# Kernel optimization log

Measured on AMD Instinct MI355X. Metric: run time of the kernel, lower is better.

Reference implementation:

```python
import jax, jax.numpy as jnp
import numpy as np

HEAD_DIM = 64
N_KV_HEADS = 4


def _rope(t, cos, sin):
    # t: (B, S, H, HD); cos/sin: (S, HD//2); interleaved (real, imag) pairs
    tr = t.astype(jnp.float32).reshape(*t.shape[:-1], -1, 2)
    xr, xi = tr[..., 0], tr[..., 1]
    c = cos[None, :, None, :]
    s = sin[None, :, None, :]
    out_r = xr * c - xi * s
    out_i = xr * s + xi * c
    return jnp.stack([out_r, out_i], axis=-1).reshape(t.shape).astype(t.dtype)


def setup_inputs() -> dict:
    key = jax.random.key(0)
    ks = jax.random.split(key, 5)
    B, S, D = 2, 2048, 1024
    kv_dim = N_KV_HEADS * HEAD_DIM  # 256
    x = jax.random.normal(ks[0], (B, S, D), jnp.float32)
    wq = jax.random.normal(ks[1], (D, D), jnp.float32) * 0.02
    wk = jax.random.normal(ks[2], (kv_dim, D), jnp.float32) * 0.02
    wv = jax.random.normal(ks[3], (kv_dim, D), jnp.float32) * 0.02
    wo = jax.random.normal(ks[4], (D, D), jnp.float32) * 0.02
    # precompute_freqs_cis (LLaMA): theta = 10000
    half = HEAD_DIM // 2
    inv_freq = 1.0 / (10000.0 ** (np.arange(0, HEAD_DIM, 2).astype(np.float32) / HEAD_DIM))
    ang = np.outer(np.arange(S, dtype=np.float32), inv_freq)  # (S, half)
    freqs_cos = jnp.asarray(np.cos(ang), jnp.float32)
    freqs_sin = jnp.asarray(np.sin(ang), jnp.float32)
    return {"x": x, "wq": wq, "wk": wk, "wv": wv, "wo": wo,
            "freqs_cos": freqs_cos, "freqs_sin": freqs_sin}


def reference(x, wq, wk, wv, wo, freqs_cos, freqs_sin):
    B, S, D = x.shape
    HD = HEAD_DIM
    HKV = N_KV_HEADS
    H = D // HD
    NREP = H // HKV
    # QKV projections (torch Linear: y = x @ W.T)
    xq = jnp.einsum('bsd,od->bso', x, wq).reshape(B, S, H, HD)
    xk = jnp.einsum('bsd,od->bso', x, wk).reshape(B, S, HKV, HD)
    xv = jnp.einsum('bsd,od->bso', x, wv).reshape(B, S, HKV, HD)
    # RoPE (complex multiply on interleaved pairs)
    xq = _rope(xq, freqs_cos, freqs_sin)
    xk = _rope(xk, freqs_cos, freqs_sin)
    # GQA: group query heads by kv head instead of materializing repeated KV
    xq = xq.reshape(B, S, HKV, NREP, HD)
    scale = 1.0 / jnp.sqrt(jnp.asarray(HD, jnp.float32))
    scores = jnp.einsum('bqkrh,bskh->bkrqs', xq, xk) * scale  # (B,HKV,NREP,S,S)
    causal = jnp.tril(jnp.ones((S, S), bool))
    scores = jnp.where(causal, scores, jnp.finfo(scores.dtype).min)
    probs = jax.nn.softmax(scores, axis=-1)
    out = jnp.einsum('bkrqs,bskh->bqkrh', probs, xv).reshape(B, S, H * HD)
    return jnp.einsum('bso,do->bsd', out, wo)
```

## Files before the change

kernel.cpp:

```cpp
#include <hip/hip_runtime.h>
#include <hip/hip_bf16.h>

typedef __attribute__((ext_vector_type(8))) short short8;
typedef __attribute__((ext_vector_type(4))) float floatx4;
typedef __attribute__((ext_vector_type(4))) float float4v;
typedef __attribute__((ext_vector_type(4))) unsigned short ushort4v;

#define S_LEN 2048
#define D_MODEL 1024
#define HD 64
#define HQ 16
#define HKV 4
#define QK_PRESCALE 0.18033688011112042f

__device__ __forceinline__ unsigned short f2bf(float f) {
    unsigned int u = __builtin_bit_cast(unsigned int, f);
    u += 0x7fffu + ((u >> 16) & 1u);
    return (unsigned short)(u >> 16);
}

__device__ __forceinline__ unsigned int cvt_pk_bf16(float lo, float hi) {
    unsigned int r;
    asm volatile("v_cvt_pk_bf16_f32 %0, %1, %2" : "=v"(r) : "v"(lo), "v"(hi));
    return r;
}

__device__ __forceinline__ float exp2_hw(float x) {
    float r;
    asm("v_exp_f32 %0, %1" : "=v"(r) : "v"(x));
    return r;
}

__device__ __forceinline__ void gload16(const unsigned short* g, unsigned short* l) {
    __builtin_amdgcn_global_load_lds(
        (const __attribute__((address_space(1))) void*)g,
        (__attribute__((address_space(3))) void*)l, 16, 0, 0);
}

__global__ void cvt_f32_bf16(const float* __restrict__ in, unsigned short* __restrict__ out, int n) {
    int i = (blockIdx.x * blockDim.x + threadIdx.x) * 4;
    int stride = gridDim.x * blockDim.x * 4;
    for (; i < n; i += stride) {
        float4v v = *(const float4v*)(in + i);
        ushort4v o;
        o.x = f2bf(v.x); o.y = f2bf(v.y); o.z = f2bf(v.z); o.w = f2bf(v.w);
        *(ushort4v*)(out + i) = o;
    }
}

__global__ void cvt_weights(const float* __restrict__ wq, const float* __restrict__ wk,
                            const float* __restrict__ wv, const float* __restrict__ wo,
                            unsigned short* __restrict__ dst) {
    int i = (blockIdx.x * blockDim.x + threadIdx.x) * 4;
    const float* src; int off;
    if (i < 1048576)      { src = wq; off = i; }
    else if (i < 1310720) { src = wk; off = i - 1048576; }
    else if (i < 1572864) { src = wv; off = i - 1310720; }
    else                  { src = wo; off = i - 1572864; }
    float4v v = *(const float4v*)(src + off);
    ushort4v o;
    o.x = f2bf(v.x); o.y = f2bf(v.y); o.z = f2bf(v.z); o.w = f2bf(v.w);
    *(ushort4v*)(dst + i) = o;
}

template<int EPI>
__global__ __launch_bounds__(256) void gemm128(
    const unsigned short* __restrict__ A, const unsigned short* __restrict__ W,
    float* __restrict__ C,
    unsigned short* __restrict__ Qb, unsigned short* __restrict__ Kb, unsigned short* __restrict__ Vtb,
    const float* __restrict__ fcos, const float* __restrict__ fsin,
    int K, int N)
{
    __shared__ __align__(16) unsigned short Asm[128 * 64];
    __shared__ __align__(16) unsigned short Bsm[128 * 64];

    const int tid  = threadIdx.x;
    const int lane = tid & 63;
    const int w    = tid >> 6;
    const int wr   = w >> 1, wc = w & 1;
    const int l15  = lane & 15, lhi = lane >> 4;
    const int row0 = blockIdx.x * 128;
    const int col0 = blockIdx.y * 128;

    const int r_in = tid >> 3;
    const int sp   = tid & 7;
    const int sl   = sp ^ (r_in & 7);

    floatx4 acc[4][4] = {};

    for (int k0 = 0; k0 < K; k0 += 64) {
        #pragma unroll
        for (int i = 0; i < 4; i++) {
            const int r = i * 32 + r_in;
            gload16(A + (size_t)(row0 + r) * K + k0 + sl * 8, Asm + i * 2048 + w * 512);
            gload16(W + (size_t)(col0 + r) * K + k0 + sl * 8, Bsm + i * 2048 + w * 512);
        }
        __syncthreads();

        short8 af[4][2], bfr[4][2];
        const int rx = l15 & 7;
        #pragma unroll
        for (int mi = 0; mi < 4; mi++) {
            const int rowa = wr * 64 + mi * 16 + l15;
            const int rowb = wc * 64 + mi * 16 + l15;
            #pragma unroll
            for (int ks = 0; ks < 2; ks++) {
                const int slot = (ks * 4 + lhi) ^ rx;
                af[mi][ks]  = *(const short8*)&Asm[rowa * 64 + slot * 8];
                bfr[mi][ks] = *(const short8*)&Bsm[rowb * 64 + slot * 8];
            }
        }

        __builtin_amdgcn_s_setprio(1);
        #pragma unroll
        for (int mi = 0; mi < 4; mi++)
        #pragma unroll
        for (int ni = 0; ni < 4; ni++) {
            acc[mi][ni] = __builtin_amdgcn_mfma_f32_16x16x32_bf16(af[mi][0], bfr[ni][0], acc[mi][ni], 0, 0, 0);
            acc[mi][ni] = __builtin_amdgcn_mfma_f32_16x16x32_bf16(af[mi][1], bfr[ni][1], acc[mi][ni], 0, 0, 0);
        }
        __builtin_amdgcn_s_setprio(0);
        __syncthreads();
    }

    #pragma unroll
    for (int mi = 0; mi < 4; mi++)
    #pragma unroll
    for (int ni = 0; ni < 4; ni++)
    #pragma unroll
    for (int j = 0; j < 4; j++) {
        const int row = row0 + wr * 64 + mi * 16 + lhi * 4 + j;
        const int col = col0 + wc * 64 + ni * 16 + l15;
        float v = acc[mi][ni][j];
        if (EPI == 0) {
            C[(size_t)row * D_MODEL + col] = v;
        } else {
            if (col0 < D_MODEL) {
                float pv = __shfl_xor(v, 1);
                int s  = row & (S_LEN - 1);
                int fi = (col & (HD - 1)) >> 1;
                float c  = fcos[s * (HD / 2) + fi];
                float sn = fsin[s * (HD / 2) + fi];
                float o = (col & 1) ? (pv * sn + v * c) : (v * c - pv * sn);
                Qb[(size_t)row * D_MODEL + col] = f2bf(o * QK_PRESCALE);
            } else if (col0 < D_MODEL + 256) {
                int ck = col - D_MODEL;
                float pv = __shfl_xor(v, 1);
                int s  = row & (S_LEN - 1);
                int fi = (ck & (HD - 1)) >> 1;
                float c  = fcos[s * (HD / 2) + fi];
                float sn = fsin[s * (HD / 2) + fi];
                float o = (ck & 1) ? (pv * sn + v * c) : (v * c - pv * sn);
                Kb[(size_t)row * 256 + ck] = f2bf(o);
            } else {
                int cv = col - (D_MODEL + 256);
                int b = row >> 11, s = row & (S_LEN - 1);
                int kvh = cv >> 6, d = cv & (HD - 1);
                Vtb[((size_t)(b * HKV + kvh) * HD + d) * S_LEN + s] = f2bf(v);
            }
        }
    }
}

__global__ __launch_bounds__(256) void flash_attn(
    const unsigned short* __restrict__ Q, const unsigned short* __restrict__ Kk,
    const unsigned short* __restrict__ Vt, unsigned short* __restrict__ O)
{
    const int tid  = threadIdx.x;
    const int lane = tid & 63;
    const int wid  = tid >> 6;
    const int l15 = lane & 15, lhi = lane >> 4;
    const int bid = blockIdx.x;
    const int h  = bid & 15;
    const int b  = (bid >> 4) & 1;
    const int qc = 63 - (bid >> 5);
    const int kvh = h >> 2;
    const int qbase = qc * 32;

    __shared__ __align__(16) unsigned short plds[4][16][72];
    __shared__ __align__(16) float Olds[3][32][64];
    __shared__ float mlds[3][2][16], llds[3][2][16];

    short8 qf[2][2];
    #pragma unroll
    for (int qi = 0; qi < 2; qi++) {
        const unsigned short* qp =
            Q + ((size_t)(b * S_LEN + qbase + qi * 16 + l15) * HQ + h) * HD + lhi * 8;
        qf[qi][0] = *(const short8*)qp;
        qf[qi][1] = *(const short8*)(qp + 32);
    }

    floatx4 oacc[2][4] = {};
    float m_run[2] = {-1e30f, -1e30f};
    float l_run[2] = {0.f, 0.f};

    const unsigned short* kbase = Kk + ((size_t)(b * S_LEN) * HKV + kvh) * HD + lhi * 8;
    const unsigned short* vbase = Vt + (size_t)((b * HKV + kvh) * HD + l15) * S_LEN + lhi * 8;

    const int nt = (qbase + 31) / 64 + 1;

    for (int t = wid; t < nt; t += 4) {
        const int s0 = t * 64;

        short8 kv[4][2];
        #pragma unroll
        for (int st = 0; st < 4; st++) {
            const unsigned short* kp = kbase + (size_t)(s0 + st * 16 + l15) * (HKV * HD);
            kv[st][0] = *(const short8*)kp;
            kv[st][1] = *(const short8*)(kp + 32);
        }

        floatx4 sacc[2][4] = {};
        __builtin_amdgcn_s_setprio(1);
        #pragma unroll
        for (int qi = 0; qi < 2; qi++)
        #pragma unroll
        for (int st = 0; st < 4; st++) {
            sacc[qi][st] = __builtin_amdgcn_mfma_f32_16x16x32_bf16(kv[st][0], qf[qi][0], sacc[qi][st], 0, 0, 0);
            sacc[qi][st] = __builtin_amdgcn_mfma_f32_16x16x32_bf16(kv[st][1], qf[qi][1], sacc[qi][st], 0, 0, 0);
        }
        __builtin_amdgcn_s_setprio(0);

        #pragma unroll
        for (int dct = 0; dct < 4; dct++) {
            const unsigned short* vp = vbase + (size_t)(dct * 16) * S_LEN + s0;
            kv[dct][0] = *(const short8*)vp;
            kv[dct][1] = *(const short8*)(vp + 32);
        }

        short8 pf[2][2];
        #pragma unroll
        for (int qi = 0; qi < 2; qi++) {
            const int qb = qbase + qi * 16;
            const int q = qb + l15;
            if (s0 + 63 > qb) {
                #pragma unroll
                for (int st = 0; st < 4; st++)
                #pragma unroll
                for (int j = 0; j < 4; j++) {
                    int s = s0 + st * 16 + lhi * 4 + j;
                    if (s > q) sacc[qi][st][j] = -1e30f;
                }
            }

            float rmax = sacc[qi][0][0];
            #pragma unroll
            for (int st = 0; st < 4; st++)
            #pragma unroll
            for (int j = 0; j < 4; j++) rmax = fmaxf(rmax, sacc[qi][st][j]);
            rmax = fmaxf(rmax, __shfl_xor(rmax, 16));
            rmax = fmaxf(rmax, __shfl_xor(rmax, 32));

            if (!__all(rmax <= m_run[qi] + 8.0f)) {
                float mnew = fmaxf(m_run[qi], rmax);
                float rr = exp2_hw(m_run[qi] - mnew);
                m_run[qi] = mnew;
                l_run[qi] *= rr;
                #pragma unroll
                for (int dct = 0; dct < 4; dct++)
                #pragma unroll
                for (int j = 0; j < 4; j++) oacc[qi][dct][j] *= rr;
            }
            const float mcur = m_run[qi];

            float psum = 0.f;
            unsigned int pk[4][2];
            #pragma unroll
            for (int st = 0; st < 4; st++) {
                float p0 = exp2_hw(sacc[qi][st][0] - mcur);
                float p1 = exp2_hw(sacc[qi][st][1] - mcur);
                float p2 = exp2_hw(sacc[qi][st][2] - mcur);
                float p3 = exp2_hw(sacc[qi][st][3] - mcur);
                psum += (p0 + p1) + (p2 + p3);
                pk[st][0] = cvt_pk_bf16(p0, p1);
                pk[st][1] = cvt_pk_bf16(p2, p3);
            }
            psum += __shfl_xor(psum, 16);
            psum += __shfl_xor(psum, 32);
            l_run[qi] += psum;

            #pragma unroll
            for (int st = 0; st < 4; st++) {
                *(unsigned int*)&plds[wid][l15][st * 16 + lhi * 4 + 0] = pk[st][0];
                *(unsigned int*)&plds[wid][l15][st * 16 + lhi * 4 + 2] = pk[st][1];
            }
            pf[qi][0] = *(const short8*)&plds[wid][l15][lhi * 8];
            pf[qi][1] = *(const short8*)&plds[wid][l15][32 + lhi * 8];
        }

        __builtin_amdgcn_s_setprio(1);
        #pragma unroll
        for (int qi = 0; qi < 2; qi++)
        #pragma unroll
        for (int dct = 0; dct < 4; dct++) {
            oacc[qi][dct] = __builtin_amdgcn_mfma_f32_16x16x32_bf16(kv[dct][0], pf[qi][0], oacc[qi][dct], 0, 0, 0);
            oacc[qi][dct] = __builtin_amdgcn_mfma_f32_16x16x32_bf16(kv[dct][1], pf[qi][1], oacc[qi][dct], 0, 0, 0);
        }
        __builtin_amdgcn_s_setprio(0);
    }

    if (wid >= 1) {
        #pragma unroll
        for (int qi = 0; qi < 2; qi++) {
            if (lhi == 0) { mlds[wid - 1][qi][l15] = m_run[qi]; llds[wid - 1][qi][l15] = l_run[qi]; }
            #pragma unroll
            for (int dct = 0; dct < 4; dct++)
            #pragma unroll
            for (int j = 0; j < 4; j++)
                Olds[wid - 1][qi * 16 + dct * 4 + j][lane] = oacc[qi][dct][j];
        }
    }
    __syncthreads();
    if (wid == 0) {
        #pragma unroll
        for (int qi = 0; qi < 2; qi++) {
            float mw0 = mlds[0][qi][l15], lw0 = llds[0][qi][l15];
            float mw1 = mlds[1][qi][l15], lw1 = llds[1][qi][l15];
            float mw2 = mlds[2][qi][l15], lw2 = llds[2][qi][l15];
            float mm = fmaxf(fmaxf(m_run[qi], mw0), fmaxf(mw1, mw2));
            float fs = exp2_hw(m_run[qi] - mm);
            float f0 = exp2_hw(mw0 - mm);
            float f1 = exp2_hw(mw1 - mm);
            float f2 = exp2_hw(mw2 - mm);
            float rl = 1.0f / (l_run[qi] * fs + lw0 * f0 + lw1 * f1 + lw2 * f2);
            fs *= rl; f0 *= rl; f1 *= rl; f2 *= rl;
            const int q = qbase + qi * 16 + l15;
            unsigned short* op = O + ((size_t)(b * S_LEN + q) * HQ + h) * HD + lhi * 4;
            #pragma unroll
            for (int dct = 0; dct < 4; dct++) {
                float o[4];
                #pragma unroll
                for (int j = 0; j < 4; j++) {
                    const int r = qi * 16 + dct * 4 + j;
                    o[j] = oacc[qi][dct][j] * fs + Olds[0][r][lane] * f0
                         + Olds[1][r][lane] * f1 + Olds[2][r][lane] * f2;
                }
                *(unsigned int*)(op + dct * 16)     = cvt_pk_bf16(o[0], o[1]);
                *(unsigned int*)(op + dct * 16 + 2) = cvt_pk_bf16(o[2], o[3]);
            }
        }
    }
}

extern "C" void kernel_launch(void* const* d_in, const int* in_sizes, int n_in,
                              void* d_out, int out_size, void* d_ws, size_t ws_size,
                              hipStream_t stream) {
    const float* x    = (const float*)d_in[0];
    const float* wq   = (const float*)d_in[1];
    const float* wk   = (const float*)d_in[2];
    const float* wv   = (const float*)d_in[3];
    const float* wo   = (const float*)d_in[4];
    const float* fcos = (const float*)d_in[5];
    const float* fsin = (const float*)d_in[6];
    float* out = (float*)d_out;

    char* ws = (char*)d_ws;
    unsigned short* xb    = (unsigned short*)(ws);
    unsigned short* wqkvb = (unsigned short*)(ws + 8388608);
    unsigned short* wob   = (unsigned short*)(ws + 11534336);
    unsigned short* Qb    = (unsigned short*)(ws + 13631488);
    unsigned short* Kb    = (unsigned short*)(ws + 22020096);
    unsigned short* Vtb   = (unsigned short*)(ws + 24117248);
    unsigned short* Ab    = (unsigned short*)(ws + 26214400);

    cvt_f32_bf16<<<1024, 256, 0, stream>>>(x, xb, 4096 * 1024);
    cvt_weights<<<2560, 256, 0, stream>>>(wq, wk, wv, wo, wqkvb);

    gemm128<1><<<dim3(32, 12), 256, 0, stream>>>(xb, wqkvb, nullptr, Qb, Kb, Vtb,
                                                 fcos, fsin, 1024, 1536);

    flash_attn<<<64 * 32, 256, 0, stream>>>(Qb, Kb, Vtb, Ab);

    gemm128<0><<<dim3(32, 8), 256, 0, stream>>>(Ab, wob, out, nullptr, nullptr, nullptr,
                                                nullptr, nullptr, 1024, 1024);
}
```

Baseline: 139.8 us.

## Share GQA K/V tiles across query-head waves via double-buffered LDS

Each block now handles one KV head with four waves, one per query head in the GQA group, instead of splitting one head's KV range across waves. K and V tiles are loaded cooperatively into swizzled, double-buffered LDS, so every loaded tile is reused by all four heads. The next tile is prefetched while the current one is being computed. The cross-wave softmax merge through LDS is removed, the grid shrinks from 2048 to 512 blocks, and query chunks are ordered so that long and short causal rows are interleaved. The cost is fewer resident waves per CU, which gives less latency hiding, plus a block-wide barrier on every KV tile.

```diff
diff --git a/kernel.cpp b/kernel.cpp
--- a/kernel.cpp
+++ b/kernel.cpp
@@ -171,15 +171,16 @@
     const int wid  = tid >> 6;
     const int l15 = lane & 15, lhi = lane >> 4;
     const int bid = blockIdx.x;
-    const int h  = bid & 15;
-    const int b  = (bid >> 4) & 1;
-    const int qc = 63 - (bid >> 5);
-    const int kvh = h >> 2;
+    const int g   = bid & 7;
+    const int b   = g >> 2, kvh = g & 3;
+    const int i   = bid >> 3;
+    const int qc  = (i < 32) ? (63 - i) : (i - 32);
+    const int h   = kvh * 4 + wid;
     const int qbase = qc * 32;
 
+    __shared__ __align__(16) unsigned short Klds[2][64 * 64];
+    __shared__ __align__(16) unsigned short Vlds[2][64 * 64];
     __shared__ __align__(16) unsigned short plds[4][16][72];
-    __shared__ __align__(16) float Olds[3][32][64];
-    __shared__ float mlds[3][2][16], llds[3][2][16];
 
     short8 qf[2][2];
     #pragma unroll
@@ -194,20 +195,53 @@
     float m_run[2] = {-1e30f, -1e30f};
     float l_run[2] = {0.f, 0.f};
 
-    const unsigned short* kbase = Kk + ((size_t)(b * S_LEN) * HKV + kvh) * HD + lhi * 8;
-    const unsigned short* vbase = Vt + (size_t)((b * HKV + kvh) * HD + l15) * S_LEN + lhi * 8;
+    const int r_st  = tid >> 3;
+    const int sl_st = tid & 7;
+    const unsigned short* ksrc = Kk + (size_t)(b * S_LEN) * 256 + kvh * 64;
+    const unsigned short* vsrc = Vt + (size_t)((b * HKV + kvh) * HD) * S_LEN;
+    const int ldsbase = (wid * 64) * 8;
 
     const int nt = (qbase + 31) / 64 + 1;
 
-    for (int t = wid; t < nt; t += 4) {
-        const int s0 = t * 64;
-
-        short8 kv[4][2];
+    {
+        const int s0 = 0;
+        #pragma unroll
+        for (int j = 0; j < 2; j++) {
+            const int r  = j * 32 + r_st;
+            const int sl = sl_st ^ (r & 7);
+            gload16(ksrc + (size_t)(s0 + r) * 256 + sl * 8,   &Klds[0][j * 2048 + ldsbase]);
+            gload16(vsrc + (size_t)r * S_LEN + s0 + sl * 8,   &Vlds[0][j * 2048 + ldsbase]);
+        }
+    }
+    asm volatile("s_waitcnt vmcnt(0)" ::: "memory");
+    __syncthreads();
+
+    const int rsw = l15 & 7;
+
+    for (int t = 0; t < nt; t++) {
+        const int s0  = t * 64;
+        const int buf = t & 1;
+
+        if (t + 1 < nt) {
+            const int s1 = s0 + 64;
+            #pragma unroll
+            for (int j = 0; j < 2; j++) {
+                const int r  = j * 32 + r_st;
+                const int sl = sl_st ^ (r & 7);
+                gload16(ksrc + (size_t)(s1 + r) * 256 + sl * 8, &Klds[buf ^ 1][j * 2048 + ldsbase]);
+                gload16(vsrc + (size_t)r * S_LEN + s1 + sl * 8, &Vlds[buf ^ 1][j * 2048 + ldsbase]);
+            }
+        }
+
+        short8 kf[4][2];
         #pragma unroll
         for (int st = 0; st < 4; st++) {
-            const unsigned short* kp = kbase + (size_t)(s0 + st * 16 + l15) * (HKV * HD);
-            kv[st][0] = *(const short8*)kp;
-            kv[st][1] = *(const short8*)(kp + 32);
+            const int row = st * 16 + l15;
+            #pragma unroll
+            for (int half = 0; half < 2; half++) {
+                const int slot = ((half << 2) | lhi) ^ rsw;
+                kf[st][half] = *(const short8*)&Klds[buf][row * 64 + slot * 8];
+            }
         }
 
         floatx4 sacc[2][4] = {};
@@ -216,16 +250,20 @@
         for (int qi = 0; qi < 2; qi++)
         #pragma unroll
         for (int st = 0; st < 4; st++) {
-            sacc[qi][st] = __builtin_amdgcn_mfma_f32_16x16x32_bf16(kv[st][0], qf[qi][0], sacc[qi][st], 0, 0, 0);
-            sacc[qi][st] = __builtin_amdgcn_mfma_f32_16x16x32_bf16(kv[st][1], qf[qi][1], sacc[qi][st], 0, 0, 0);
+            sacc[qi][st] = __builtin_amdgcn_mfma_f32_16x16x32_bf16(kf[st][0], qf[qi][0], sacc[qi][st], 0, 0, 0);
+            sacc[qi][st] = __builtin_amdgcn_mfma_f32_16x16x32_bf16(kf[st][1], qf[qi][1], sacc[qi][st], 0, 0, 0);
         }
         __builtin_amdgcn_s_setprio(0);
 
+        short8 vf[4][2];
         #pragma unroll
         for (int dct = 0; dct < 4; dct++) {
-            const unsigned short* vp = vbase + (size_t)(dct * 16) * S_LEN + s0;
-            kv[dct][0] = *(const short8*)vp;
-            kv[dct][1] = *(const short8*)(vp + 32);
+            const int row = dct * 16 + l15;
+            #pragma unroll
+            for (int half = 0; half < 2; half++) {
+                const int slot = ((half << 2) | lhi) ^ rsw;
+                vf[dct][half] = *(const short8*)&Vlds[buf][row * 64 + slot * 8];
+            }
         }
 
         short8 pf[2][2];
@@ -293,51 +331,26 @@
         for (int qi = 0; qi < 2; qi++)
         #pragma unroll
         for (int dct = 0; dct < 4; dct++) {
-            oacc[qi][dct] = __builtin_amdgcn_mfma_f32_16x16x32_bf16(kv[dct][0], pf[qi][0], oacc[qi][dct], 0, 0, 0);
-            oacc[qi][dct] = __builtin_amdgcn_mfma_f32_16x16x32_bf16(kv[dct][1], pf[qi][1], oacc[qi][dct], 0, 0, 0);
+            oacc[qi][dct] = __builtin_amdgcn_mfma_f32_16x16x32_bf16(vf[dct][0], pf[qi][0], oacc[qi][dct], 0, 0, 0);
+            oacc[qi][dct] = __builtin_amdgcn_mfma_f32_16x16x32_bf16(vf[dct][1], pf[qi][1], oacc[qi][dct], 0, 0, 0);
         }
         __builtin_amdgcn_s_setprio(0);
-    }
-
-    if (wid >= 1) {
-        #pragma unroll
-        for (int qi = 0; qi < 2; qi++) {
-            if (lhi == 0) { mlds[wid - 1][qi][l15] = m_run[qi]; llds[wid - 1][qi][l15] = l_run[qi]; }
-            #pragma unroll
-            for (int dct = 0; dct < 4; dct++)
-            #pragma unroll
-            for (int j = 0; j < 4; j++)
-                Olds[wid - 1][qi * 16 + dct * 4 + j][lane] = oacc[qi][dct][j];
-        }
-    }
-    __syncthreads();
-    if (wid == 0) {
-        #pragma unroll
-        for (int qi = 0; qi < 2; qi++) {
-            float mw0 = mlds[0][qi][l15], lw0 = llds[0][qi][l15];
-            float mw1 = mlds[1][qi][l15], lw1 = llds[1][qi][l15];
-            float mw2 = mlds[2][qi][l15], lw2 = llds[2][qi][l15];
-            float mm = fmaxf(fmaxf(m_run[qi], mw0), fmaxf(mw1, mw2));
-            float fs = exp2_hw(m_run[qi] - mm);
-            float f0 = exp2_hw(mw0 - mm);
-            float f1 = exp2_hw(mw1 - mm);
-            float f2 = exp2_hw(mw2 - mm);
-            float rl = 1.0f / (l_run[qi] * fs + lw0 * f0 + lw1 * f1 + lw2 * f2);
-            fs *= rl; f0 *= rl; f1 *= rl; f2 *= rl;
-            const int q = qbase + qi * 16 + l15;
-            unsigned short* op = O + ((size_t)(b * S_LEN + q) * HQ + h) * HD + lhi * 4;
-            #pragma unroll
-            for (int dct = 0; dct < 4; dct++) {
-                float o[4];
-                #pragma unroll
-                for (int j = 0; j < 4; j++) {
-                    const int r = qi * 16 + dct * 4 + j;
-                    o[j] = oacc[qi][dct][j] * fs + Olds[0][r][lane] * f0
-                         + Olds[1][r][lane] * f1 + Olds[2][r][lane] * f2;
-                }
-                *(unsigned int*)(op + dct * 16)     = cvt_pk_bf16(o[0], o[1]);
-                *(unsigned int*)(op + dct * 16 + 2) = cvt_pk_bf16(o[2], o[3]);
-            }
+
+        asm volatile("s_waitcnt vmcnt(0)" ::: "memory");
+        __syncthreads();
+    }
+
+    #pragma unroll
+    for (int qi = 0; qi < 2; qi++) {
+        float rl = 1.0f / l_run[qi];
+        const int q = qbase + qi * 16 + l15;
+        unsigned short* op = O + ((size_t)(b * S_LEN + q) * HQ + h) * HD + lhi * 4;
+        #pragma unroll
+        for (int dct = 0; dct < 4; dct++) {
+            unsigned int w0 = cvt_pk_bf16(oacc[qi][dct][0] * rl, oacc[qi][dct][1] * rl);
+            unsigned int w1 = cvt_pk_bf16(oacc[qi][dct][2] * rl, oacc[qi][dct][3] * rl);
+            *(unsigned int*)(op + dct * 16)     = w0;
+            *(unsigned int*)(op + dct * 16 + 2) = w1;
         }
     }
 }
@@ -369,7 +382,7 @@
     gemm128<1><<<dim3(32, 12), 256, 0, stream>>>(xb, wqkvb, nullptr, Qb, Kb, Vtb,
                                                  fcos, fsin, 1024, 1536);
 
-    flash_attn<<<64 * 32, 256, 0, stream>>>(Qb, Kb, Vtb, Ab);
+    flash_attn<<<512, 256, 0, stream>>>(Qb, Kb, Vtb, Ab);
 
     gemm128<0><<<dim3(32, 8), 256, 0, stream>>>(Ab, wob, out, nullptr, nullptr, nullptr,
                                                 nullptr, nullptr, 1024, 1024);
```

New measurement: 126.5 us. 1.11x faster.
